# Optimization experiments

Hardware: AMD Instinct MI355X
Metric: run time of the kernel (lower is better)

Reference implementation:

```python
import jax, jax.numpy as jnp
import numpy as np

FEAT = 4      # feature_dim
INFO = 8      # info_dim
B, U, A = 128, 16, 1024  # batch, num_users, num_ris_antennas


def setup_inputs() -> dict:
    key = jax.random.key(0)
    ks = jax.random.split(key, 7)
    channel = jax.random.normal(ks[0], (B, FEAT, U, A), dtype=jnp.float32)
    # layer 1: four branches (ll, lg, gl, gg), each Conv2d(4, 8, 1) -> W:[Cin,Cout]
    W1 = jax.random.normal(ks[1], (4, FEAT, INFO), dtype=jnp.float32) * 0.3
    b1 = jax.random.normal(ks[2], (4, INFO), dtype=jnp.float32) * 0.01
    # layers 2..7: four branches each Conv2d(32, 8, 1)
    Wm = jax.random.normal(ks[3], (6, 4, 4 * INFO, INFO), dtype=jnp.float32) * 0.15
    bm = jax.random.normal(ks[4], (6, 4, INFO), dtype=jnp.float32) * 0.01
    # layer 8: Conv2d(32, 1, 1)
    W8 = jax.random.normal(ks[5], (4 * INFO, 1), dtype=jnp.float32) * 0.15
    b8 = jax.random.normal(ks[6], (1,), dtype=jnp.float32) * 0.01
    return {"channel": channel, "W1": W1, "b1": b1, "Wm": Wm, "bm": bm,
            "W8": W8, "b8": b8}


def _conv1x1(x, W, b):
    # x: [B, Cin, U, A], W: [Cin, Cout], b: [Cout]
    return jnp.einsum('bcua,co->boua', x, W) + b[None, :, None, None]


def _process(x, W, b, e_u, e_a):
    # W: [4, Cin, INFO], b: [4, INFO]; branches: ll, lg, gl, gg
    f_ll = jax.nn.relu(_conv1x1(x, W[0], b[0]))
    f_lg = jnp.einsum('boua,ax->boux', jax.nn.relu(_conv1x1(x, W[1], b[1])), e_a)
    f_gl = jnp.einsum('uv,bova->boua', e_u, jax.nn.relu(_conv1x1(x, W[2], b[2])))
    gg = jnp.einsum('uv,bova->boua', e_u, jax.nn.relu(_conv1x1(x, W[3], b[3])))
    f_gg = jnp.einsum('boua,ax->boux', gg, e_a)
    return jnp.concatenate([f_ll, f_lg, f_gl, f_gg], axis=1)


def reference(channel, W1, b1, Wm, bm, W8, b8):
    _, _, nu, na = channel.shape
    # global_info flags True -> uniform averaging matrices ones/N
    e_u = jnp.full((nu, nu), 1.0 / nu, dtype=channel.dtype)
    e_a = jnp.full((na, na), 1.0 / na, dtype=channel.dtype)

    f = _process(channel, W1, b1, e_u, e_a)
    f1 = f                                      # skip 1
    f = _process(f, Wm[0], bm[0], e_u, e_a)     # layer 2
    f = _process(f, Wm[1], bm[1], e_u, e_a)     # layer 3
    f3 = f                                      # skip 3
    f = _process(f, Wm[2], bm[2], e_u, e_a)     # layer 4
    f = _process(f, Wm[3], bm[3], e_u, e_a)     # layer 5
    f = (f + f1) / 2
    f = _process(f, Wm[4], bm[4], e_u, e_a)     # layer 6
    f = _process(f, Wm[5], bm[5], e_u, e_a)     # layer 7
    f = (f + f3) / 2
    out = _conv1x1(f, W8, b8).mean(axis=2) * jnp.pi   # mean over users -> [B, 1, A]
    return out
```

## Files before the change

### kernel.cpp

```cpp
#include <hip/hip_runtime.h>


#define NB 128
#define NU 16
#define NA 1024

typedef float v2f __attribute__((ext_vector_type(2)));
typedef __attribute__((ext_vector_type(8))) short bf16x8;
typedef __attribute__((ext_vector_type(16))) float f32x16;

static constexpr float PI_F = 3.14159265358979323846f;

__device__ __forceinline__ void pk_fma_acc(v2f& acc, v2f a, v2f b) {
    asm("v_pk_fma_f32 %0, %1, %2, %0" : "+v"(acc) : "v"(a), "v"(b));
}
__device__ __forceinline__ unsigned int cvtpk(float a, float b) {
    unsigned int r;
    asm("v_cvt_pk_bf16_f32 %0, %1, %2" : "=v"(r) : "v"(a), "v"(b));
    return r;
}
__device__ __forceinline__ void unpack8(uint4 v, float x[8]) {
    x[0] = __uint_as_float(v.x << 16); x[1] = __uint_as_float(v.x & 0xffff0000u);
    x[2] = __uint_as_float(v.y << 16); x[3] = __uint_as_float(v.y & 0xffff0000u);
    x[4] = __uint_as_float(v.z << 16); x[5] = __uint_as_float(v.z & 0xffff0000u);
    x[6] = __uint_as_float(v.w << 16); x[7] = __uint_as_float(v.w & 0xffff0000u);
}
__device__ __forceinline__ void store8f(unsigned short* p, const float y[8]) {
    uint4 v;
    v.x = cvtpk(y[0], y[1]); v.y = cvtpk(y[2], y[3]);
    v.z = cvtpk(y[4], y[5]); v.w = cvtpk(y[6], y[7]);
    *reinterpret_cast<uint4*>(p) = v;
}
__device__ __forceinline__ float treesum16(f32x16 v) {
    float a0 = v[0] + v[1], a1 = v[2] + v[3], a2 = v[4] + v[5], a3 = v[6] + v[7];
    float a4 = v[8] + v[9], a5 = v[10] + v[11], a6 = v[12] + v[13], a7 = v[14] + v[15];
    float b0 = a0 + a1, b1 = a2 + a3, b2 = a4 + a5, b3 = a6 + a7;
    return (b0 + b1) + (b2 + b3);
}

__device__ __forceinline__ float merge3v(const v2f* y, int lane) {
    float w[4];
    const bool s0 = (lane & 1) != 0;
#pragma unroll
    for (int k = 0; k < 4; ++k) {
        float lo = s0 ? y[k].y : y[k].x;
        float hi = s0 ? y[k].x : y[k].y;
        w[k] = lo + __shfl_xor(hi, 1, 64);
    }
    const bool s1 = (lane & 2) != 0;
#pragma unroll
    for (int k = 0; k < 2; ++k) {
        float lo = s1 ? w[2 * k + 1] : w[2 * k];
        float hi = s1 ? w[2 * k] : w[2 * k + 1];
        w[k] = lo + __shfl_xor(hi, 2, 64);
    }
    const bool s2 = (lane & 4) != 0;
    float lo = s2 ? w[1] : w[0];
    float hi = s2 ? w[0] : w[1];
    return lo + __shfl_xor(hi, 4, 64);
}

template <int NZ>
__global__ __launch_bounds__(128) void layer_first_t(
    const float* __restrict__ ch, const float* __restrict__ W1,
    const float* __restrict__ b1, unsigned short* __restrict__ ll_out,
    float* __restrict__ lg_out, float* __restrict__ gl_out,
    float* __restrict__ gg_out)
{
    constexpr int UN = NU / NZ;
    const int b = blockIdx.x;
    const int a = blockIdx.y * 128 + threadIdx.x;
    const int uz = blockIdx.z;
    const int lane = threadIdx.x & 63;
    const int tid = threadIdx.x;

    __shared__ float s_lg[UN][8];
    __shared__ float s_gg[8];
    for (int t = tid; t < UN * 8; t += 128) s_lg[t >> 3][t & 7] = 0.f;
    if (tid >= 64 && tid < 72) s_gg[tid & 7] = 0.f;
    __syncthreads();

    v2f glacc2[4], ggacc2[4];
#pragma unroll
    for (int i = 0; i < 4; ++i) { glacc2[i] = v2f{0.f, 0.f}; ggacc2[i] = v2f{0.f, 0.f}; }

#pragma unroll
    for (int k = 0; k < UN; ++k) {
        const int u = uz * UN + k;
        float x[4];
#pragma unroll
        for (int c = 0; c < 4; ++c)
            x[c] = ch[(((size_t)b * 4 + c) * NU + u) * NA + a];

        v2f y2[16];
        const v2f* b2 = reinterpret_cast<const v2f*>(b1);
#pragma unroll
        for (int o = 0; o < 16; ++o) y2[o] = b2[o];
#pragma unroll
        for (int c = 0; c < 4; ++c) {
            const v2f xx = v2f{x[c], x[c]};
#pragma unroll
            for (int j = 0; j < 4; ++j) {
                const v2f* wr = reinterpret_cast<const v2f*>(W1 + (j * 4 + c) * 8);
#pragma unroll
                for (int oi = 0; oi < 4; ++oi)
                    pk_fma_acc(y2[j * 4 + oi], xx, wr[oi]);
            }
        }
#pragma unroll
        for (int o = 0; o < 16; ++o)
            y2[o] = v2f{__builtin_fmaxf(y2[o].x, 0.f), __builtin_fmaxf(y2[o].y, 0.f)};

        const size_t xoff = (((size_t)(b * NU + u)) * NA + a) * 8;
        {
            uint4 v;
            v.x = cvtpk(y2[0].x, y2[0].y); v.y = cvtpk(y2[1].x, y2[1].y);
            v.z = cvtpk(y2[2].x, y2[2].y); v.w = cvtpk(y2[3].x, y2[3].y);
            *reinterpret_cast<uint4*>(ll_out + xoff) = v;
        }
#pragma unroll
        for (int i = 0; i < 4; ++i) {
            glacc2[i] += y2[8 + i];
            ggacc2[i] += y2[12 + i];
        }
        float lr = merge3v(y2 + 4, lane);
        atomicAdd(&s_lg[k][lane & 7], lr);
    }
    {
        const float invU = 1.f / 16.f;
        float ga[8];
#pragma unroll
        for (int i = 0; i < 4; ++i) { ga[2*i] = glacc2[i].x; ga[2*i+1] = glacc2[i].y; }
#pragma unroll
        for (int c = 0; c < 8; ++c)
            gl_out[(((size_t)uz * NB + b) * 8 + c) * NA + a] = ga[c] * invU;
    }
    float gga[8];
#pragma unroll
    for (int i = 0; i < 4; ++i) { gga[2*i] = ggacc2[i].x; gga[2*i+1] = ggacc2[i].y; }
    float gr = merge3v(reinterpret_cast<const v2f*>(gga), lane);
    atomicAdd(&s_gg[lane & 7], gr);
    __syncthreads();
    for (int t = tid; t < UN * 8; t += 128)
        atomicAdd(lg_out + ((size_t)b * NU + uz * UN + (t >> 3)) * 8 + (t & 7),
                  s_lg[t >> 3][t & 7]);
    if (tid >= 64 && tid < 72)
        atomicAdd(gg_out + b * 8 + (tid & 7), s_gg[tid & 7]);
}

__global__ __launch_bounds__(256) void prep_base_k(
    const float* __restrict__ lg_sum, const float* __restrict__ lg_skip,
    const float* __restrict__ gg_sum, const float* __restrict__ gg_skip,
    const float* __restrict__ Wl, const float* __restrict__ bl,
    float* __restrict__ base)
{
    const int t = blockIdx.x * 256 + threadIdx.x;
    if (t >= NB * NU) return;
    const int b = t >> 4;
    const float invA = 1.f / 1024.f, invUA = 1.f / 16384.f;
    float lg[8], gg[8];
#pragma unroll
    for (int c = 0; c < 8; ++c) {
        float v = lg_sum[t * 8 + c] * invA;
        if (lg_skip) v = (v + lg_skip[t * 8 + c] * invA) * 0.5f;
        lg[c] = v;
    }
#pragma unroll
    for (int c = 0; c < 8; ++c) {
        float v = gg_sum[b * 8 + c] * invUA;
        if (gg_skip) v = (v + gg_skip[b * 8 + c] * invUA) * 0.5f;
        gg[c] = v;
    }
    float y[32];
#pragma unroll
    for (int o = 0; o < 32; ++o) y[o] = bl[o];
#pragma unroll
    for (int j = 0; j < 4; ++j)
#pragma unroll
        for (int c = 0; c < 8; ++c) {
            const float* wl = Wl + (j * 32 + 8 + c) * 8;
            const float* wg = Wl + (j * 32 + 24 + c) * 8;
#pragma unroll
            for (int oi = 0; oi < 8; ++oi) {
                y[j * 8 + oi] = fmaf(lg[c], wl[oi], y[j * 8 + oi]);
                y[j * 8 + oi] = fmaf(gg[c], wg[oi], y[j * 8 + oi]);
            }
        }
#pragma unroll
    for (int o = 0; o < 32; ++o) base[t * 32 + o] = y[o];
}

template <int NZ>
__global__ __launch_bounds__(64) void layer_main_t(
    const unsigned short* ll_in, const float* __restrict__ gl_in,
    const float* __restrict__ gl_skip, const float* __restrict__ base,
    const float* __restrict__ Wl,
    const unsigned short* __restrict__ ll_skip,
    const float* __restrict__ ch, const float* __restrict__ W1,
    const float* __restrict__ b1,
    unsigned short* ll_out, float* __restrict__ lg_out,
    float* __restrict__ gl_out, float* __restrict__ gg_out)
{
    constexpr int UN = NU / NZ;
    const int b = blockIdx.x;
    const int lane = threadIdx.x;
    const int o = lane & 31;
    const int h4 = 4 * (lane >> 5);
    const int half = lane >> 5;
    const int a32 = blockIdx.y * 32 + o;
    const int uz = blockIdx.z;
    const bool lohalf = lane < 32;

    __shared__ float s_lg[UN][8];
    __shared__ float s_gg[8];
    __shared__ float myl[8 * 68];
    for (int t = lane; t < UN * 8; t += 64) s_lg[t >> 3][t & 7] = 0.f;
    if (lane < 8) s_gg[lane] = 0.f;
    __syncthreads();

    const int jbr = o >> 3, oi = o & 7;

    bf16x8 Bfrag;
    {
        unsigned int t4[4];
#pragma unroll
        for (int r = 0; r < 4; ++r) {
            float w0 = Wl[(jbr * 32 + 2 * r) * 8 + oi];
            float w1 = Wl[(jbr * 32 + 2 * r + 1) * 8 + oi];
            float h0 = __uint_as_float(cvtpk(w0, w0) << 16);
            float h1 = __uint_as_float(cvtpk(w1, w1) << 16);
            t4[r] = cvtpk(lohalf ? w0 : (w0 - h0), lohalf ? w1 : (w1 - h1));
        }
        uint4 bw = make_uint4(t4[0], t4[1], t4[2], t4[3]);
        Bfrag = __builtin_bit_cast(bf16x8, bw);
    }

    float g[8];
#pragma unroll
    for (int c = 0; c < 8; ++c) {
        float s = 0.f;
#pragma unroll
        for (int z = 0; z < NZ; ++z)
            s += gl_in[(((size_t)z * NB + b) * 8 + c) * NA + a32];
        g[c] = s;
    }
    if (gl_skip) {
#pragma unroll
        for (int c = 0; c < 8; ++c) {
            float s = 0.f;
#pragma unroll
            for (int z = 0; z < NZ; ++z)
                s += gl_skip[(((size_t)z * NB + b) * 8 + c) * NA + a32];
            g[c] = (g[c] + s) * 0.5f;
        }
    }

    f32x16 cT;
    {
        bf16x8 Ag, Bh, Br;
        {
            unsigned int t4[4];
#pragma unroll
            for (int r = 0; r < 4; ++r) {
                float g0 = g[2 * r], g1 = g[2 * r + 1];
                float h0 = __uint_as_float(cvtpk(g0, g0) << 16);
                float h1 = __uint_as_float(cvtpk(g1, g1) << 16);
                t4[r] = cvtpk(lohalf ? g0 : (g0 - h0), lohalf ? g1 : (g1 - h1));
            }
            uint4 u = make_uint4(t4[0], t4[1], t4[2], t4[3]);
            Ag = __builtin_bit_cast(bf16x8, u);
        }
        {
            unsigned int th[4], tr[4];
#pragma unroll
            for (int r = 0; r < 4; ++r) {
                float w0 = Wl[(jbr * 32 + 16 + 2 * r) * 8 + oi];
                float w1 = Wl[(jbr * 32 + 16 + 2 * r + 1) * 8 + oi];
                float h0 = __uint_as_float(cvtpk(w0, w0) << 16);
                float h1 = __uint_as_float(cvtpk(w1, w1) << 16);
                th[r] = cvtpk(w0, w1);
                tr[r] = cvtpk(w0 - h0, w1 - h1);
            }
            uint4 uh = make_uint4(th[0], th[1], th[2], th[3]);
            uint4 ur = make_uint4(tr[0], tr[1], tr[2], tr[3]);
            Bh = __builtin_bit_cast(bf16x8, uh);
            Br = __builtin_bit_cast(bf16x8, ur);
        }
        f32x16 z16;
#pragma unroll
        for (int r = 0; r < 16; ++r) z16[r] = 0.f;
        cT = __builtin_amdgcn_mfma_f32_32x32x16_bf16(Ag, Bh, z16, 0, 0, 0);
        cT = __builtin_amdgcn_mfma_f32_32x32x16_bf16(Ag, Br, cT, 0, 0, 0);
    }

    f32x16 acc;
#pragma unroll
    for (int r = 0; r < 16; ++r) acc[r] = 0.f;

    const unsigned short* llrow =
        ll_in + (((size_t)(b * NU + uz * UN + half)) * NA + a32) * 8;
    const size_t pstride = (size_t)2 * NA * 8;
    uint4 xv = *reinterpret_cast<const uint4*>(llrow);

#pragma unroll
    for (int kp = 0; kp < UN / 2; ++kp) {
        const int u0 = uz * UN + 2 * kp;
        uint4 xnext = xv;
        if (kp + 1 < UN / 2)
            xnext = *reinterpret_cast<const uint4*>(llrow + (size_t)(kp + 1) * pstride);

        const float bse0 = base[(b * NU + u0) * 32 + o];
        const float bse1 = base[(b * NU + u0 + 1) * 32 + o];

        uint4 xs;
        xs.x = (unsigned)__shfl_xor((int)xv.x, 32, 64);
        xs.y = (unsigned)__shfl_xor((int)xv.y, 32, 64);
        xs.z = (unsigned)__shfl_xor((int)xv.z, 32, 64);
        xs.w = (unsigned)__shfl_xor((int)xv.w, 32, 64);
        uint4 a0u, a1u;
        a0u.x = lohalf ? xv.x : xs.x; a0u.y = lohalf ? xv.y : xs.y;
        a0u.z = lohalf ? xv.z : xs.z; a0u.w = lohalf ? xv.w : xs.w;
        a1u.x = lohalf ? xs.x : xv.x; a1u.y = lohalf ? xs.y : xv.y;
        a1u.z = lohalf ? xs.z : xv.z; a1u.w = lohalf ? xs.w : xv.w;
        bf16x8 A0 = __builtin_bit_cast(bf16x8, a0u);
        bf16x8 A1 = __builtin_bit_cast(bf16x8, a1u);

        f32x16 d0 = __builtin_amdgcn_mfma_f32_32x32x16_bf16(A0, Bfrag, cT, 0, 0, 0);
        f32x16 d1 = __builtin_amdgcn_mfma_f32_32x32x16_bf16(A1, Bfrag, cT, 0, 0, 0);
#pragma unroll
        for (int r = 0; r < 16; ++r) {
            d0[r] = __builtin_fmaxf(d0[r] + bse0, 0.f);
            d1[r] = __builtin_fmaxf(d1[r] + bse1, 0.f);
        }

        float red0 = treesum16(d0);
        red0 += __shfl_xor(red0, 32, 64);
        if (lane >= 8 && lane < 16) atomicAdd(&s_lg[2 * kp][lane - 8], red0);
        float red1 = treesum16(d1);
        red1 += __shfl_xor(red1, 32, 64);
        if (lane >= 8 && lane < 16) atomicAdd(&s_lg[2 * kp + 1][lane - 8], red1);

#pragma unroll
        for (int r = 0; r < 16; ++r) acc[r] += d0[r] + d1[r];

        if (o < 8) {
#pragma unroll
            for (int q = 0; q < 4; ++q) {
                *reinterpret_cast<float4*>(&myl[o * 68 + q * 8 + h4]) =
                    make_float4(d0[4*q], d0[4*q+1], d0[4*q+2], d0[4*q+3]);
                *reinterpret_cast<float4*>(&myl[o * 68 + 32 + q * 8 + h4]) =
                    make_float4(d1[4*q], d1[4*q+1], d1[4*q+2], d1[4*q+3]);
            }
        }
        __syncthreads();
        float y[8];
#pragma unroll
        for (int c = 0; c < 8; ++c) y[c] = myl[c * 68 + lane];

        const int u_lane = u0 + half;
        const size_t xoff = (((size_t)(b * NU + u_lane)) * NA + a32) * 8;
        if (ll_skip) {
            float s[8];
            unpack8(*reinterpret_cast<const uint4*>(ll_skip + xoff), s);
#pragma unroll
            for (int c = 0; c < 8; ++c) y[c] = (y[c] + s[c]) * 0.5f;
        } else if (ch) {
            float xc[4];
#pragma unroll
            for (int c = 0; c < 4; ++c)
                xc[c] = ch[(((size_t)b * 4 + c) * NU + u_lane) * NA + a32];
            float s[8];
#pragma unroll
            for (int i = 0; i < 8; ++i) s[i] = b1[i];
#pragma unroll
            for (int c = 0; c < 4; ++c)
#pragma unroll
                for (int i = 0; i < 8; ++i)
                    s[i] = fmaf(xc[c], W1[c * 8 + i], s[i]);
#pragma unroll
            for (int i = 0; i < 8; ++i)
                y[i] = (y[i] + __builtin_fmaxf(s[i], 0.f)) * 0.5f;
        }
        store8f(ll_out + xoff, y);
        __syncthreads();
        xv = xnext;
    }

    float gr = treesum16(acc);
    gr += __shfl_xor(gr, 32, 64);
    if (lane >= 24 && lane < 32) atomicAdd(&s_gg[lane - 24], gr);

    if (o >= 16 && o < 24) {
        const float invU = 1.f / 16.f;
        float* gp = gl_out + (((size_t)uz * NB + b) * 8 + (o - 16)) * NA
                  + blockIdx.y * 32;
#pragma unroll
        for (int q = 0; q < 4; ++q)
            *reinterpret_cast<float4*>(gp + q * 8 + h4) =
                make_float4(acc[4*q]*invU, acc[4*q+1]*invU, acc[4*q+2]*invU, acc[4*q+3]*invU);
    }
    __syncthreads();
    for (int t = lane; t < UN * 8; t += 64)
        atomicAdd(lg_out + ((size_t)b * NU + uz * UN + (t >> 3)) * 8 + (t & 7),
                  s_lg[t >> 3][t & 7]);
    if (lane < 8)
        atomicAdd(gg_out + b * 8 + lane, s_gg[lane]);
}

template <int NZ>
__global__ __launch_bounds__(128) void layer_out_t(
    const unsigned short* __restrict__ ll,
    const float* __restrict__ lg7, const float* __restrict__ lg3,
    const float* __restrict__ gl7, const float* __restrict__ gl3,
    const float* __restrict__ gg7, const float* __restrict__ gg3,
    const float* __restrict__ W8, const float* __restrict__ b8,
    float* __restrict__ out)
{
    constexpr int UN = NU / NZ;
    const int b = blockIdx.x;
    const int a = blockIdx.y * 128 + threadIdx.x;
    const int uz = blockIdx.z;
    const float invA = 1.f / 1024.f, invUA = 1.f / 16384.f, invU = 1.f / 16.f;

    float acc = 0.f;
#pragma unroll
    for (int k = 0; k < UN; ++k) {
        const int u = uz * UN + k;
        float x[8];
        unpack8(*reinterpret_cast<const uint4*>(
            ll + (((size_t)(b * NU + u)) * NA + a) * 8), x);
#pragma unroll
        for (int c = 0; c < 8; ++c) acc += x[c] * W8[c];
    }
    acc *= invU;

    if (uz == 0) {
        float sb = b8[0];
#pragma unroll
        for (int c = 0; c < 8; ++c) {
            float s7 = 0.f, s3 = 0.f;
#pragma unroll
            for (int u = 0; u < NU; ++u) {
                s7 += lg7[(b * NU + u) * 8 + c];
                s3 += lg3[(b * NU + u) * 8 + c];
            }
            sb += ((s7 * invA + s3 * invA) * 0.5f * invU) * W8[8 + c];
        }
#pragma unroll
        for (int c = 0; c < 8; ++c)
            sb += ((gg7[b * 8 + c] + gg3[b * 8 + c]) * invUA * 0.5f) * W8[24 + c];

        float s7[8], s3[8];
#pragma unroll
        for (int i = 0; i < 8; ++i) { s7[i] = 0.f; s3[i] = 0.f; }
#pragma unroll
        for (int z = 0; z < NZ; ++z)
#pragma unroll
            for (int i = 0; i < 8; ++i) {
                s7[i] += gl7[(((size_t)z * NB + b) * 8 + i) * NA + a];
                s3[i] += gl3[(((size_t)z * NB + b) * 8 + i) * NA + a];
            }
#pragma unroll
        for (int i = 0; i < 8; ++i)
            acc += 0.5f * (s7[i] + s3[i]) * W8[16 + i];
        acc += sb;
    }
    atomicAdd(out + (size_t)b * NA + a, acc * PI_F);
}

static constexpr size_t LLsz = (size_t)NB * NU * NA * 8;
static constexpr size_t GLsz = (size_t)NB * NA * 8;
static constexpr size_t LGsz = (size_t)NB * NU * 8;
static constexpr size_t GGsz = (size_t)NB * 8;

template <int NZ>
static void run_pipeline(const float* channel, const float* W1, const float* b1,
                         const float* Wm, const float* bm, const float* W8,
                         const float* b8, float* out, int out_bytes,
                         void* d_ws, hipStream_t stream)
{
    unsigned short* cur = (unsigned short*)d_ws;
    unsigned short* f3s = cur + LLsz;
    float* glb = (float*)(f3s + LLsz);
    float* g0 = glb;
    float* g1 = glb + (size_t)NZ * GLsz;
    float* g2 = glb + (size_t)2 * NZ * GLsz;
    float* g3 = glb + (size_t)3 * NZ * GLsz;
    float* lgb = glb + (size_t)4 * NZ * GLsz;
    float* ggb = lgb + 7 * LGsz;
    float* base = ggb + 7 * GGsz;

    hipMemsetAsync(lgb, 0, (7 * LGsz + 7 * GGsz) * sizeof(float), stream);
    hipMemsetAsync(out, 0, out_bytes, stream);

    dim3 gridF(NB, NA / 128, NZ), blkF(128);
    dim3 gridM(NB, NA / 32, NZ), blkM(64);

    layer_first_t<NZ><<<gridF, blkF, 0, stream>>>(channel, W1, b1, cur, lgb, g0, ggb);

    prep_base_k<<<8, 256, 0, stream>>>(lgb, nullptr, ggb, nullptr, Wm, bm, base);
    layer_main_t<NZ><<<gridM, blkM, 0, stream>>>(cur, g0, nullptr, base, Wm,
        nullptr, nullptr, nullptr, nullptr,
        cur, lgb + 1 * LGsz, g2, ggb + 1 * GGsz);

    prep_base_k<<<8, 256, 0, stream>>>(lgb + 1 * LGsz, nullptr, ggb + 1 * GGsz, nullptr,
                                       Wm + 1024, bm + 32, base);
    layer_main_t<NZ><<<gridM, blkM, 0, stream>>>(cur, g2, nullptr, base, Wm + 1024,
        nullptr, nullptr, nullptr, nullptr,
        f3s, lgb + 2 * LGsz, g1, ggb + 2 * GGsz);

    prep_base_k<<<8, 256, 0, stream>>>(lgb + 2 * LGsz, nullptr, ggb + 2 * GGsz, nullptr,
                                       Wm + 2048, bm + 64, base);
    layer_main_t<NZ><<<gridM, blkM, 0, stream>>>(f3s, g1, nullptr, base, Wm + 2048,
        nullptr, nullptr, nullptr, nullptr,
        cur, lgb + 3 * LGsz, g3, ggb + 3 * GGsz);

    prep_base_k<<<8, 256, 0, stream>>>(lgb + 3 * LGsz, nullptr, ggb + 3 * GGsz, nullptr,
                                       Wm + 3072, bm + 96, base);
    layer_main_t<NZ><<<gridM, blkM, 0, stream>>>(cur, g3, nullptr, base, Wm + 3072,
        nullptr, channel, W1, b1,
        cur, lgb + 4 * LGsz, g2, ggb + 4 * GGsz);

    prep_base_k<<<8, 256, 0, stream>>>(lgb + 4 * LGsz, lgb, ggb + 4 * GGsz, ggb,
                                       Wm + 4096, bm + 128, base);
    layer_main_t<NZ><<<gridM, blkM, 0, stream>>>(cur, g2, g0, base, Wm + 4096,
        nullptr, nullptr, nullptr, nullptr,
        cur, lgb + 5 * LGsz, g3, ggb + 5 * GGsz);

    prep_base_k<<<8, 256, 0, stream>>>(lgb + 5 * LGsz, nullptr, ggb + 5 * GGsz, nullptr,
                                       Wm + 5120, bm + 160, base);
    layer_main_t<NZ><<<gridM, blkM, 0, stream>>>(cur, g3, nullptr, base, Wm + 5120,
        f3s, nullptr, nullptr, nullptr,
        cur, lgb + 6 * LGsz, g2, ggb + 6 * GGsz);

    layer_out_t<NZ><<<gridF, blkF, 0, stream>>>(cur, lgb + 6 * LGsz, lgb + 2 * LGsz,
                                                g2, g1, ggb + 6 * GGsz, ggb + 2 * GGsz,
                                                W8, b8, out);
}

static size_t ws_req(int nz) {
    return LLsz * 2 * sizeof(unsigned short)
         + (size_t)4 * nz * GLsz * sizeof(float)
         + (7 * LGsz + 7 * GGsz + 2048 * 32) * sizeof(float);
}

extern "C" void kernel_launch(void* const* d_in, const int* in_sizes, int n_in,
                              void* d_out, int out_size, void* d_ws, size_t ws_size,
                              hipStream_t stream) {
    const float* channel = (const float*)d_in[0];
    const float* W1 = (const float*)d_in[1];
    const float* b1 = (const float*)d_in[2];
    const float* Wm = (const float*)d_in[3];
    const float* bm = (const float*)d_in[4];
    const float* W8 = (const float*)d_in[5];
    const float* b8 = (const float*)d_in[6];
    float* out = (float*)d_out;

    if (ws_size >= ws_req(2)) {
        run_pipeline<2>(channel, W1, b1, Wm, bm, W8, b8, out, out_size, d_ws, stream);
    } else {
        run_pipeline<1>(channel, W1, b1, Wm, bm, W8, b8, out, out_size, d_ws, stream);
    }
}
```

Measured before the change: 331.8 us.

## Use MFMA in first layer and fuse output projection into last main layer

Rewrites the first layer to compute the four 1x1 conv branches with a bf16 MFMA using a hi/lo split of inputs and weights, replacing packed FP32 FMAs, with an LDS transpose for the ll output. It also folds the final W8 dot product into the last main layer, which accumulates per-position partials into a workspace buffer instead of writing the bf16 ll tensor. That removes one full ll write and read, and the output kernel becomes a light finisher. The cost is extra LDS syncs in the first layer and atomics into the new partial buffer.

Measured after the change: 340.3 us. +2.5%, slower.

```diff
diff --git a/kernel.cpp b/kernel.cpp
--- a/kernel.cpp
+++ b/kernel.cpp
@@ -11,13 +11,13 @@
 
 static constexpr float PI_F = 3.14159265358979323846f;
 
-__device__ __forceinline__ void pk_fma_acc(v2f& acc, v2f a, v2f b) {
-    asm("v_pk_fma_f32 %0, %1, %2, %0" : "+v"(acc) : "v"(a), "v"(b));
-}
 __device__ __forceinline__ unsigned int cvtpk(float a, float b) {
     unsigned int r;
     asm("v_cvt_pk_bf16_f32 %0, %1, %2" : "=v"(r) : "v"(a), "v"(b));
     return r;
+}
+__device__ __forceinline__ float bf16hi(float x) {
+    return __uint_as_float(cvtpk(x, x) << 16);
 }
 __device__ __forceinline__ void unpack8(uint4 v, float x[8]) {
     x[0] = __uint_as_float(v.x << 16); x[1] = __uint_as_float(v.x & 0xffff0000u);
@@ -38,30 +38,8 @@
     return (b0 + b1) + (b2 + b3);
 }
 
-__device__ __forceinline__ float merge3v(const v2f* y, int lane) {
-    float w[4];
-    const bool s0 = (lane & 1) != 0;
-#pragma unroll
-    for (int k = 0; k < 4; ++k) {
-        float lo = s0 ? y[k].y : y[k].x;
-        float hi = s0 ? y[k].x : y[k].y;
-        w[k] = lo + __shfl_xor(hi, 1, 64);
-    }
-    const bool s1 = (lane & 2) != 0;
-#pragma unroll
-    for (int k = 0; k < 2; ++k) {
-        float lo = s1 ? w[2 * k + 1] : w[2 * k];
-        float hi = s1 ? w[2 * k] : w[2 * k + 1];
-        w[k] = lo + __shfl_xor(hi, 2, 64);
-    }
-    const bool s2 = (lane & 4) != 0;
-    float lo = s2 ? w[1] : w[0];
-    float hi = s2 ? w[0] : w[1];
-    return lo + __shfl_xor(hi, 4, 64);
-}
-
 template <int NZ>
-__global__ __launch_bounds__(128) void layer_first_t(
+__global__ __launch_bounds__(64) void layer_first_t(
     const float* __restrict__ ch, const float* __restrict__ W1,
     const float* __restrict__ b1, unsigned short* __restrict__ ll_out,
     float* __restrict__ lg_out, float* __restrict__ gl_out,
@@ -69,83 +47,139 @@
 {
     constexpr int UN = NU / NZ;
     const int b = blockIdx.x;
-    const int a = blockIdx.y * 128 + threadIdx.x;
+    const int lane = threadIdx.x;
+    const int o = lane & 31;
+    const int h4 = 4 * (lane >> 5);
+    const int half = lane >> 5;
+    const int a32 = blockIdx.y * 32 + o;
     const int uz = blockIdx.z;
-    const int lane = threadIdx.x & 63;
-    const int tid = threadIdx.x;
+    const bool lohalf = lane < 32;
 
     __shared__ float s_lg[UN][8];
     __shared__ float s_gg[8];
-    for (int t = tid; t < UN * 8; t += 128) s_lg[t >> 3][t & 7] = 0.f;
-    if (tid >= 64 && tid < 72) s_gg[tid & 7] = 0.f;
+    __shared__ float myl[8 * 68];
+    for (int t = lane; t < UN * 8; t += 64) s_lg[t >> 3][t & 7] = 0.f;
+    if (lane < 8) s_gg[lane] = 0.f;
     __syncthreads();
 
-    v2f glacc2[4], ggacc2[4];
-#pragma unroll
-    for (int i = 0; i < 4; ++i) { glacc2[i] = v2f{0.f, 0.f}; ggacc2[i] = v2f{0.f, 0.f}; }
-
-#pragma unroll
-    for (int k = 0; k < UN; ++k) {
-        const int u = uz * UN + k;
-        float x[4];
-#pragma unroll
-        for (int c = 0; c < 4; ++c)
-            x[c] = ch[(((size_t)b * 4 + c) * NU + u) * NA + a];
-
-        v2f y2[16];
-        const v2f* b2 = reinterpret_cast<const v2f*>(b1);
-#pragma unroll
-        for (int o = 0; o < 16; ++o) y2[o] = b2[o];
+    const int jbr = o >> 3, oi = o & 7;
+
+    bf16x8 Bfrag;
+    {
+        float wh[4], wr[4];
 #pragma unroll
         for (int c = 0; c < 4; ++c) {
-            const v2f xx = v2f{x[c], x[c]};
-#pragma unroll
-            for (int j = 0; j < 4; ++j) {
-                const v2f* wr = reinterpret_cast<const v2f*>(W1 + (j * 4 + c) * 8);
-#pragma unroll
-                for (int oi = 0; oi < 4; ++oi)
-                    pk_fma_acc(y2[j * 4 + oi], xx, wr[oi]);
-            }
-        }
-#pragma unroll
-        for (int o = 0; o < 16; ++o)
-            y2[o] = v2f{__builtin_fmaxf(y2[o].x, 0.f), __builtin_fmaxf(y2[o].y, 0.f)};
-
-        const size_t xoff = (((size_t)(b * NU + u)) * NA + a) * 8;
+            float w = W1[(jbr * 4 + c) * 8 + oi];
+            wh[c] = bf16hi(w);
+            wr[c] = w - wh[c];
+        }
+        uint4 bw = make_uint4(cvtpk(wh[0], wh[1]), cvtpk(wh[2], wh[3]),
+                              cvtpk(wr[0], wr[1]), cvtpk(wr[2], wr[3]));
+        Bfrag = __builtin_bit_cast(bf16x8, bw);
+    }
+    f32x16 cT;
+    {
+        const float bb = b1[o];
+#pragma unroll
+        for (int r = 0; r < 16; ++r) cT[r] = bb;
+    }
+
+    f32x16 acc;
+#pragma unroll
+    for (int r = 0; r < 16; ++r) acc[r] = 0.f;
+
+#pragma unroll
+    for (int kp = 0; kp < UN / 2; ++kp) {
+        const int u0 = uz * UN + 2 * kp;
+        const int u_lane = u0 + half;
+
+        float xc[4], xo[4];
+#pragma unroll
+        for (int c = 0; c < 4; ++c) {
+            xc[c] = ch[(((size_t)b * 4 + c) * NU + u_lane) * NA + a32];
+            xo[c] = __shfl_xor(xc[c], 32, 64);
+        }
+        float x0[4], x1[4];
+#pragma unroll
+        for (int c = 0; c < 4; ++c) {
+            x0[c] = lohalf ? xc[c] : xo[c];
+            x1[c] = lohalf ? xo[c] : xc[c];
+        }
+        bf16x8 A0, A1;
         {
-            uint4 v;
-            v.x = cvtpk(y2[0].x, y2[0].y); v.y = cvtpk(y2[1].x, y2[1].y);
-            v.z = cvtpk(y2[2].x, y2[2].y); v.w = cvtpk(y2[3].x, y2[3].y);
-            *reinterpret_cast<uint4*>(ll_out + xoff) = v;
-        }
-#pragma unroll
-        for (int i = 0; i < 4; ++i) {
-            glacc2[i] += y2[8 + i];
-            ggacc2[i] += y2[12 + i];
-        }
-        float lr = merge3v(y2 + 4, lane);
-        atomicAdd(&s_lg[k][lane & 7], lr);
-    }
-    {
+            float v[4];
+#pragma unroll
+            for (int c = 0; c < 4; ++c) {
+                float h = bf16hi(x0[c]);
+                v[c] = lohalf ? h : (x0[c] - h);
+            }
+            unsigned t0 = cvtpk(v[0], v[1]), t1 = cvtpk(v[2], v[3]);
+            uint4 u = make_uint4(t0, t1, t0, t1);
+            A0 = __builtin_bit_cast(bf16x8, u);
+#pragma unroll
+            for (int c = 0; c < 4; ++c) {
+                float h = bf16hi(x1[c]);
+                v[c] = lohalf ? h : (x1[c] - h);
+            }
+            t0 = cvtpk(v[0], v[1]); t1 = cvtpk(v[2], v[3]);
+            u = make_uint4(t0, t1, t0, t1);
+            A1 = __builtin_bit_cast(bf16x8, u);
+        }
+
+        f32x16 d0 = __builtin_amdgcn_mfma_f32_32x32x16_bf16(A0, Bfrag, cT, 0, 0, 0);
+        f32x16 d1 = __builtin_amdgcn_mfma_f32_32x32x16_bf16(A1, Bfrag, cT, 0, 0, 0);
+#pragma unroll
+        for (int r = 0; r < 16; ++r) {
+            d0[r] = __builtin_fmaxf(d0[r], 0.f);
+            d1[r] = __builtin_fmaxf(d1[r], 0.f);
+        }
+
+        float red0 = treesum16(d0);
+        red0 += __shfl_xor(red0, 32, 64);
+        if (lane >= 8 && lane < 16) atomicAdd(&s_lg[2 * kp][lane - 8], red0);
+        float red1 = treesum16(d1);
+        red1 += __shfl_xor(red1, 32, 64);
+        if (lane >= 8 && lane < 16) atomicAdd(&s_lg[2 * kp + 1][lane - 8], red1);
+
+#pragma unroll
+        for (int r = 0; r < 16; ++r) acc[r] += d0[r] + d1[r];
+
+        if (o < 8) {
+#pragma unroll
+            for (int q = 0; q < 4; ++q) {
+                *reinterpret_cast<float4*>(&myl[o * 68 + q * 8 + h4]) =
+                    make_float4(d0[4*q], d0[4*q+1], d0[4*q+2], d0[4*q+3]);
+                *reinterpret_cast<float4*>(&myl[o * 68 + 32 + q * 8 + h4]) =
+                    make_float4(d1[4*q], d1[4*q+1], d1[4*q+2], d1[4*q+3]);
+            }
+        }
+        __syncthreads();
+        float y[8];
+#pragma unroll
+        for (int c = 0; c < 8; ++c) y[c] = myl[c * 68 + lane];
+        store8f(ll_out + (((size_t)(b * NU + u_lane)) * NA + a32) * 8, y);
+        __syncthreads();
+    }
+
+    float gr = treesum16(acc);
+    gr += __shfl_xor(gr, 32, 64);
+    if (lane >= 24 && lane < 32) atomicAdd(&s_gg[lane - 24], gr);
+
+    if (o >= 16 && o < 24) {
         const float invU = 1.f / 16.f;
-        float ga[8];
-#pragma unroll
-        for (int i = 0; i < 4; ++i) { ga[2*i] = glacc2[i].x; ga[2*i+1] = glacc2[i].y; }
-#pragma unroll
-        for (int c = 0; c < 8; ++c)
-            gl_out[(((size_t)uz * NB + b) * 8 + c) * NA + a] = ga[c] * invU;
-    }
-    float gga[8];
-#pragma unroll
-    for (int i = 0; i < 4; ++i) { gga[2*i] = ggacc2[i].x; gga[2*i+1] = ggacc2[i].y; }
-    float gr = merge3v(reinterpret_cast<const v2f*>(gga), lane);
-    atomicAdd(&s_gg[lane & 7], gr);
+        float* gp = gl_out + (((size_t)uz * NB + b) * 8 + (o - 16)) * NA
+                  + blockIdx.y * 32;
+#pragma unroll
+        for (int q = 0; q < 4; ++q)
+            *reinterpret_cast<float4*>(gp + q * 8 + h4) =
+                make_float4(acc[4*q]*invU, acc[4*q+1]*invU, acc[4*q+2]*invU, acc[4*q+3]*invU);
+    }
     __syncthreads();
-    for (int t = tid; t < UN * 8; t += 128)
+    for (int t = lane; t < UN * 8; t += 64)
         atomicAdd(lg_out + ((size_t)b * NU + uz * UN + (t >> 3)) * 8 + (t & 7),
                   s_lg[t >> 3][t & 7]);
-    if (tid >= 64 && tid < 72)
-        atomicAdd(gg_out + b * 8 + (tid & 7), s_gg[tid & 7]);
+    if (lane < 8)
+        atomicAdd(gg_out + b * 8 + lane, s_gg[lane]);
 }
 
 __global__ __launch_bounds__(256) void prep_base_k(
@@ -199,7 +233,8 @@
     const float* __restrict__ ch, const float* __restrict__ W1,
     const float* __restrict__ b1,
     unsigned short* ll_out, float* __restrict__ lg_out,
-    float* __restrict__ gl_out, float* __restrict__ gg_out)
+    float* __restrict__ gl_out, float* __restrict__ gg_out,
+    const float* __restrict__ W8v, float* __restrict__ out_part)
 {
     constexpr int UN = NU / NZ;
     const int b = blockIdx.x;
@@ -227,8 +262,7 @@
         for (int r = 0; r < 4; ++r) {
             float w0 = Wl[(jbr * 32 + 2 * r) * 8 + oi];
             float w1 = Wl[(jbr * 32 + 2 * r + 1) * 8 + oi];
-            float h0 = __uint_as_float(cvtpk(w0, w0) << 16);
-            float h1 = __uint_as_float(cvtpk(w1, w1) << 16);
+            float h0 = bf16hi(w0), h1 = bf16hi(w1);
             t4[r] = cvtpk(lohalf ? w0 : (w0 - h0), lohalf ? w1 : (w1 - h1));
         }
         uint4 bw = make_uint4(t4[0], t4[1], t4[2], t4[3]);
@@ -263,8 +297,7 @@
 #pragma unroll
             for (int r = 0; r < 4; ++r) {
                 float g0 = g[2 * r], g1 = g[2 * r + 1];
-                float h0 = __uint_as_float(cvtpk(g0, g0) << 16);
-                float h1 = __uint_as_float(cvtpk(g1, g1) << 16);
+                float h0 = bf16hi(g0), h1 = bf16hi(g1);
                 t4[r] = cvtpk(lohalf ? g0 : (g0 - h0), lohalf ? g1 : (g1 - h1));
             }
             uint4 u = make_uint4(t4[0], t4[1], t4[2], t4[3]);
@@ -276,8 +309,7 @@
             for (int r = 0; r < 4; ++r) {
                 float w0 = Wl[(jbr * 32 + 16 + 2 * r) * 8 + oi];
                 float w1 = Wl[(jbr * 32 + 16 + 2 * r + 1) * 8 + oi];
-                float h0 = __uint_as_float(cvtpk(w0, w0) << 16);
-                float h1 = __uint_as_float(cvtpk(w1, w1) << 16);
+                float h0 = bf16hi(w0), h1 = bf16hi(w1);
                 th[r] = cvtpk(w0, w1);
                 tr[r] = cvtpk(w0 - h0, w1 - h1);
             }
@@ -296,6 +328,7 @@
     f32x16 acc;
 #pragma unroll
     for (int r = 0; r < 16; ++r) acc[r] = 0.f;
+    float p8 = 0.f;
 
     const unsigned short* llrow =
         ll_in + (((size_t)(b * NU + uz * UN + half)) * NA + a32) * 8;
@@ -381,9 +414,21 @@
             for (int i = 0; i < 8; ++i)
                 y[i] = (y[i] + __builtin_fmaxf(s[i], 0.f)) * 0.5f;
         }
-        store8f(ll_out + xoff, y);
+        if (W8v) {
+            float d = 0.f;
+#pragma unroll
+            for (int c = 0; c < 8; ++c) d = fmaf(y[c], W8v[c], d);
+            p8 += d;
+        } else {
+            store8f(ll_out + xoff, y);
+        }
         __syncthreads();
         xv = xnext;
+    }
+
+    if (W8v) {
+        p8 += __shfl_xor(p8, 32, 64);
+        if (lohalf) atomicAdd(&out_part[(size_t)b * NA + a32], p8);
     }
 
     float gr = treesum16(acc);
@@ -408,64 +453,46 @@
 }
 
 template <int NZ>
-__global__ __launch_bounds__(128) void layer_out_t(
-    const unsigned short* __restrict__ ll,
+__global__ __launch_bounds__(128) void layer_out_fin(
+    const float* __restrict__ outp,
     const float* __restrict__ lg7, const float* __restrict__ lg3,
     const float* __restrict__ gl7, const float* __restrict__ gl3,
     const float* __restrict__ gg7, const float* __restrict__ gg3,
     const float* __restrict__ W8, const float* __restrict__ b8,
     float* __restrict__ out)
 {
-    constexpr int UN = NU / NZ;
     const int b = blockIdx.x;
     const int a = blockIdx.y * 128 + threadIdx.x;
-    const int uz = blockIdx.z;
     const float invA = 1.f / 1024.f, invUA = 1.f / 16384.f, invU = 1.f / 16.f;
 
-    float acc = 0.f;
-#pragma unroll
-    for (int k = 0; k < UN; ++k) {
-        const int u = uz * UN + k;
-        float x[8];
-        unpack8(*reinterpret_cast<const uint4*>(
-            ll + (((size_t)(b * NU + u)) * NA + a) * 8), x);
-#pragma unroll
-        for (int c = 0; c < 8; ++c) acc += x[c] * W8[c];
-    }
-    acc *= invU;
-
-    if (uz == 0) {
-        float sb = b8[0];
-#pragma unroll
-        for (int c = 0; c < 8; ++c) {
-            float s7 = 0.f, s3 = 0.f;
-#pragma unroll
-            for (int u = 0; u < NU; ++u) {
-                s7 += lg7[(b * NU + u) * 8 + c];
-                s3 += lg3[(b * NU + u) * 8 + c];
-            }
-            sb += ((s7 * invA + s3 * invA) * 0.5f * invU) * W8[8 + c];
-        }
-#pragma unroll
-        for (int c = 0; c < 8; ++c)
-            sb += ((gg7[b * 8 + c] + gg3[b * 8 + c]) * invUA * 0.5f) * W8[24 + c];
-
-        float s7[8], s3[8];
-#pragma unroll
-        for (int i = 0; i < 8; ++i) { s7[i] = 0.f; s3[i] = 0.f; }
-#pragma unroll
-        for (int z = 0; z < NZ; ++z)
-#pragma unroll
-            for (int i = 0; i < 8; ++i) {
-                s7[i] += gl7[(((size_t)z * NB + b) * 8 + i) * NA + a];
-                s3[i] += gl3[(((size_t)z * NB + b) * 8 + i) * NA + a];
-            }
-#pragma unroll
-        for (int i = 0; i < 8; ++i)
-            acc += 0.5f * (s7[i] + s3[i]) * W8[16 + i];
-        acc += sb;
-    }
-    atomicAdd(out + (size_t)b * NA + a, acc * PI_F);
+    float acc = outp[(size_t)b * NA + a] * invU;
+
+    float sb = b8[0];
+#pragma unroll
+    for (int c = 0; c < 8; ++c) {
+        float s7 = 0.f, s3 = 0.f;
+#pragma unroll
+        for (int u = 0; u < NU; ++u) {
+            s7 += lg7[(b * NU + u) * 8 + c];
+            s3 += lg3[(b * NU + u) * 8 + c];
+        }
+        sb += ((s7 * invA + s3 * invA) * 0.5f * invU) * W8[8 + c];
+    }
+#pragma unroll
+    for (int c = 0; c < 8; ++c)
+        sb += ((gg7[b * 8 + c] + gg3[b * 8 + c]) * invUA * 0.5f) * W8[24 + c];
+
+#pragma unroll
+    for (int i = 0; i < 8; ++i) {
+        float s7 = 0.f, s3 = 0.f;
+#pragma unroll
+        for (int z = 0; z < NZ; ++z) {
+            s7 += gl7[(((size_t)z * NB + b) * 8 + i) * NA + a];
+            s3 += gl3[(((size_t)z * NB + b) * 8 + i) * NA + a];
+        }
+        acc += 0.5f * (s7 + s3) * W8[16 + i];
+    }
+    out[(size_t)b * NA + a] = (acc + sb) * PI_F;
 }
 
 static constexpr size_t LLsz = (size_t)NB * NU * NA * 8;
@@ -489,59 +516,60 @@
     float* lgb = glb + (size_t)4 * NZ * GLsz;
     float* ggb = lgb + 7 * LGsz;
     float* base = ggb + 7 * GGsz;
+    float* outp = base + 2048 * 32;
 
     hipMemsetAsync(lgb, 0, (7 * LGsz + 7 * GGsz) * sizeof(float), stream);
-    hipMemsetAsync(out, 0, out_bytes, stream);
-
-    dim3 gridF(NB, NA / 128, NZ), blkF(128);
+    hipMemsetAsync(outp, 0, (size_t)NB * NA * sizeof(float), stream);
+
     dim3 gridM(NB, NA / 32, NZ), blkM(64);
-
-    layer_first_t<NZ><<<gridF, blkF, 0, stream>>>(channel, W1, b1, cur, lgb, g0, ggb);
+    dim3 gridO(NB, NA / 128), blkO(128);
+
+    layer_first_t<NZ><<<gridM, blkM, 0, stream>>>(channel, W1, b1, cur, lgb, g0, ggb);
 
     prep_base_k<<<8, 256, 0, stream>>>(lgb, nullptr, ggb, nullptr, Wm, bm, base);
     layer_main_t<NZ><<<gridM, blkM, 0, stream>>>(cur, g0, nullptr, base, Wm,
         nullptr, nullptr, nullptr, nullptr,
-        cur, lgb + 1 * LGsz, g2, ggb + 1 * GGsz);
+        cur, lgb + 1 * LGsz, g2, ggb + 1 * GGsz, nullptr, nullptr);
 
     prep_base_k<<<8, 256, 0, stream>>>(lgb + 1 * LGsz, nullptr, ggb + 1 * GGsz, nullptr,
                                        Wm + 1024, bm + 32, base);
     layer_main_t<NZ><<<gridM, blkM, 0, stream>>>(cur, g2, nullptr, base, Wm + 1024,
         nullptr, nullptr, nullptr, nullptr,
-        f3s, lgb + 2 * LGsz, g1, ggb + 2 * GGsz);
+        f3s, lgb + 2 * LGsz, g1, ggb + 2 * GGsz, nullptr, nullptr);
 
     prep_base_k<<<8, 256, 0, stream>>>(lgb + 2 * LGsz, nullptr, ggb + 2 * GGsz, nullptr,
                                        Wm + 2048, bm + 64, base);
     layer_main_t<NZ><<<gridM, blkM, 0, stream>>>(f3s, g1, nullptr, base, Wm + 2048,
         nullptr, nullptr, nullptr, nullptr,
-        cur, lgb + 3 * LGsz, g3, ggb + 3 * GGsz);
+        cur, lgb + 3 * LGsz, g3, ggb + 3 * GGsz, nullptr, nullptr);
 
     prep_base_k<<<8, 256, 0, stream>>>(lgb + 3 * LGsz, nullptr, ggb + 3 * GGsz, nullptr,
                                        Wm + 3072, bm + 96, base);
     layer_main_t<NZ><<<gridM, blkM, 0, stream>>>(cur, g3, nullptr, base, Wm + 3072,
         nullptr, channel, W1, b1,
-        cur, lgb + 4 * LGsz, g2, ggb + 4 * GGsz);
+        cur, lgb + 4 * LGsz, g2, ggb + 4 * GGsz, nullptr, nullptr);
 
     prep_base_k<<<8, 256, 0, stream>>>(lgb + 4 * LGsz, lgb, ggb + 4 * GGsz, ggb,
                                        Wm + 4096, bm + 128, base);
     layer_main_t<NZ><<<gridM, blkM, 0, stream>>>(cur, g2, g0, base, Wm + 4096,
         nullptr, nullptr, nullptr, nullptr,
-        cur, lgb + 5 * LGsz, g3, ggb + 5 * GGsz);
+        cur, lgb + 5 * LGsz, g3, ggb + 5 * GGsz, nullptr, nullptr);
 
     prep_base_k<<<8, 256, 0, stream>>>(lgb + 5 * LGsz, nullptr, ggb + 5 * GGsz, nullptr,
                                        Wm + 5120, bm + 160, base);
     layer_main_t<NZ><<<gridM, blkM, 0, stream>>>(cur, g3, nullptr, base, Wm + 5120,
         f3s, nullptr, nullptr, nullptr,
-        cur, lgb + 6 * LGsz, g2, ggb + 6 * GGsz);
-
-    layer_out_t<NZ><<<gridF, blkF, 0, stream>>>(cur, lgb + 6 * LGsz, lgb + 2 * LGsz,
-                                                g2, g1, ggb + 6 * GGsz, ggb + 2 * GGsz,
-                                                W8, b8, out);
+        cur, lgb + 6 * LGsz, g2, ggb + 6 * GGsz, W8, outp);
+
+    layer_out_fin<NZ><<<gridO, blkO, 0, stream>>>(outp, lgb + 6 * LGsz, lgb + 2 * LGsz,
+                                                  g2, g1, ggb + 6 * GGsz, ggb + 2 * GGsz,
+                                                  W8, b8, out);
 }
 
 static size_t ws_req(int nz) {
     return LLsz * 2 * sizeof(unsigned short)
          + (size_t)4 * nz * GLsz * sizeof(float)
-         + (7 * LGsz + 7 * GGsz + 2048 * 32) * sizeof(float);
+         + (7 * LGsz + 7 * GGsz + 2048 * 32 + (size_t)NB * NA) * sizeof(float);
 }
 
 extern "C" void kernel_launch(void* const* d_in, const int* in_sizes, int n_in,
```
